# Performance work log

Hardware: AMD Instinct MI355X
Metric: run time of the kernel (lower is better)

The kernel has to match this reference:

```python
import jax, jax.numpy as jnp
import numpy as np

SCALE = 1.0
DENSE = 4
ITERS = 5


def setup_inputs() -> dict:
    key = jax.random.key(0)
    k1, k2, k3 = jax.random.split(key, 3)
    N, C, H, W = 32, 3, 512, 512
    data = jax.random.uniform(k1, (N, C, H, W), dtype=jnp.float32)
    # marginal attention distributions along x (width) and y (height); strictly positive
    attx = jax.random.uniform(k2, (N, W, 1), dtype=jnp.float32) + 1e-3
    atty = jax.random.uniform(k3, (N, H, 1), dtype=jnp.float32) + 1e-3
    return {"data": data, "attx": attx, "atty": atty}


def _iterative_clip(ax, ay, out_size, dense, iters):
    # ax, ay: (N, A) positive marginals. Normalize so each sums to out_size,
    # then iteratively clip peaks to a threshold and redistribute the clipped
    # mass uniformly (the mobula AttSamplerGrid iterative refinement).
    A = ax.shape[1]
    ax = ax / jnp.sum(ax, 1, keepdims=True) * out_size
    ay = ay / jnp.sum(ay, 1, keepdims=True) * out_size
    thr0 = jnp.float32(dense * out_size / A)
    for i in range(iters):
        t = jnp.minimum(jnp.max(ax, 1, keepdims=True), jnp.max(ay, 1, keepdims=True))
        if i == 0:
            t = jnp.minimum(t, thr0)
        ax = jnp.minimum(ax, t)
        ay = jnp.minimum(ay, t)
        ax = ax + (out_size - jnp.sum(ax, 1, keepdims=True)) / A
        ay = ay + (out_size - jnp.sum(ay, 1, keepdims=True)) / A
    return ax, ay


def _inverse_cdf(att, out_size):
    # att: (N, A) density summing (approximately) to out_size.
    # For each of out_size equally-spaced mass targets, find the fractional
    # source index p (piecewise-linear inverse of the cumulative sum), then
    # map p in [0, A] to a normalized grid coordinate in [-1, 1].
    N, A = att.shape
    c = jnp.cumsum(att, axis=1)                               # (N, A)
    step = c[:, -1] / out_size                                # ~1.0 per output pixel
    t = (jnp.arange(out_size, dtype=att.dtype) + 0.5) * step[:, None]  # (N, out)
    j = jax.vmap(lambda cr, tr: jnp.searchsorted(cr, tr, side="left"))(c, t)
    j = jnp.clip(j, 0, A - 1)
    c_prev = jnp.where(j > 0, jnp.take_along_axis(c, jnp.maximum(j - 1, 0), 1), 0.0)
    dens = jnp.take_along_axis(c, j, 1) - c_prev              # = att[n, j]
    p = j.astype(att.dtype) + (t - c_prev) / jnp.maximum(dens, 1e-6)
    return 2.0 * p / A - 1.0                                  # (N, out) in [-1, 1]


def _grid_sample_bilinear(data, grid):
    # data: (N, C, H, W); grid: (N, Ho, Wo, 2) with grid[...,0]=x, grid[...,1]=y
    # in [-1, 1]; bilinear, align_corners=True, border clamp (grid stays in range).
    N, C, H, W = data.shape
    ix = (grid[..., 0] + 1.0) * 0.5 * (W - 1)
    iy = (grid[..., 1] + 1.0) * 0.5 * (H - 1)
    x0 = jnp.floor(ix)
    y0 = jnp.floor(iy)
    wx = ix - x0
    wy = iy - y0
    x0i = jnp.clip(x0.astype(jnp.int32), 0, W - 1)
    x1i = jnp.clip(x0i + 1, 0, W - 1)
    y0i = jnp.clip(y0.astype(jnp.int32), 0, H - 1)
    y1i = jnp.clip(y0i + 1, 0, H - 1)

    def sample_one(img, x0i, x1i, y0i, y1i, wx, wy):
        # img: (C, H, W); index arrays: (Ho, Wo) -> gathers are (C, Ho, Wo)
        v00 = img[:, y0i, x0i]
        v01 = img[:, y0i, x1i]
        v10 = img[:, y1i, x0i]
        v11 = img[:, y1i, x1i]
        top = v00 * (1.0 - wx) + v01 * wx
        bot = v10 * (1.0 - wx) + v11 * wx
        return top * (1.0 - wy) + bot * wy

    return jax.vmap(sample_one)(data, x0i, x1i, y0i, y1i, wx, wy)


def reference(data, attx, atty):
    N, C, H, W = data.shape
    out_size = int(H * SCALE)
    ax, ay = _iterative_clip(attx[:, :, 0], atty[:, :, 0], out_size, DENSE, ITERS)
    px = _inverse_cdf(ax, out_size)   # x coords, vary along width
    py = _inverse_cdf(ay, out_size)   # y coords, vary along height
    gx = jnp.broadcast_to(px[:, None, :], (N, out_size, out_size))
    gy = jnp.broadcast_to(py[:, :, None], (N, out_size, out_size))
    grid = jnp.stack([gx, gy], axis=3)            # (N, Ho, Wo, 2)
    sampled = _grid_sample_bilinear(data, grid)   # (N, C, Ho, Wo)
    return sampled, grid
```

## Files before the change

### kernel.cpp

```cpp
#include <hip/hip_runtime.h>

#define NB   32
#define NC   3
#define HH   512
#define WW   512
#define AA   512
#define OUT  512

__device__ __forceinline__ float wave_sum(float v) {
#pragma unroll
    for (int m = 32; m > 0; m >>= 1) v += __shfl_xor(v, m, 64);
    return v;
}
__device__ __forceinline__ float wave_max(float v) {
#pragma unroll
    for (int m = 32; m > 0; m >>= 1) v = fmaxf(v, __shfl_xor(v, m, 64));
    return v;
}

__device__ __forceinline__ float block_sum(float v, float* red, int tid) {
    v = wave_sum(v);
    if ((tid & 63) == 0) red[tid >> 6] = v;
    __syncthreads();
    float r = red[0];
#pragma unroll
    for (int k = 1; k < 8; ++k) r += red[k];
    __syncthreads();
    return r;
}
__device__ __forceinline__ float block_max(float v, float* red, int tid) {
    v = wave_max(v);
    if ((tid & 63) == 0) red[tid >> 6] = v;
    __syncthreads();
    float r = red[0];
#pragma unroll
    for (int k = 1; k < 8; ++k) r = fmaxf(r, red[k]);
    __syncthreads();
    return r;
}

__global__ __launch_bounds__(512) void clip_cdf_kernel(
    const float* __restrict__ attx, const float* __restrict__ atty,
    float* __restrict__ px, float* __restrict__ py)
{
    __shared__ float red[8];
    __shared__ float cs[AA];

    const int n   = blockIdx.x;
    const int tid = threadIdx.x;

    float ax = attx[n * AA + tid];
    float ay = atty[n * AA + tid];

    float sx = block_sum(ax, red, tid);
    float sy = block_sum(ay, red, tid);
    ax = ax / sx * (float)OUT;
    ay = ay / sy * (float)OUT;

#pragma unroll
    for (int it = 0; it < 5; ++it) {
        float mx = block_max(ax, red, tid);
        float my = block_max(ay, red, tid);
        float tv = fminf(mx, my);
        if (it == 0) tv = fminf(tv, 4.0f);
        ax = fminf(ax, tv);
        ay = fminf(ay, tv);
        float sax = block_sum(ax, red, tid);
        float say = block_sum(ay, red, tid);
        ax += ((float)OUT - sax) * (1.0f / (float)AA);
        ay += ((float)OUT - say) * (1.0f / (float)AA);
    }

#pragma unroll
    for (int which = 0; which < 2; ++which) {
        float v = (which == 0) ? ax : ay;
        cs[tid] = v;
        __syncthreads();
#pragma unroll
        for (int off = 1; off < AA; off <<= 1) {
            float add = (tid >= off) ? cs[tid - off] : 0.0f;
            __syncthreads();
            cs[tid] += add;
            __syncthreads();
        }
        float total = cs[AA - 1];
        float step  = total / (float)OUT;
        float tk    = ((float)tid + 0.5f) * step;

        int lo = 0, hi = AA;
        while (lo < hi) {
            int mid = (lo + hi) >> 1;
            if (cs[mid] < tk) lo = mid + 1; else hi = mid;
        }
        int j = lo; if (j > AA - 1) j = AA - 1;
        float cprev = (j > 0) ? cs[j - 1] : 0.0f;
        float dens  = cs[j] - cprev;
        float p     = (float)j + (tk - cprev) / fmaxf(dens, 1e-6f);
        float g     = 2.0f * p / (float)AA - 1.0f;
        if (which == 0) px[n * OUT + tid] = g;
        else            py[n * OUT + tid] = g;
        __syncthreads();
    }
}

__global__ __launch_bounds__(256) void sample_kernel(
    const float* __restrict__ data, const float* __restrict__ px,
    const float* __restrict__ py, float* __restrict__ sampled,
    float2* __restrict__ grid)
{
    __shared__ float lrow[6][WW];

    const int bid = blockIdx.x;
    const int n   = bid >> 9;
    const int i   = bid & (OUT - 1);

    const float gy  = py[n * OUT + i];
    const float iy  = (gy + 1.0f) * 0.5f * (float)(HH - 1);
    const float y0f = floorf(iy);
    const float wy  = iy - y0f;
    int y0 = (int)y0f;
    y0 = max(0, min(y0, HH - 1));
    const int y1 = min(y0 + 1, HH - 1);

    const float* dbase = data + (size_t)n * NC * HH * WW;

#pragma unroll
    for (int k = 0; k < 3; ++k) {
        const int idx = threadIdx.x + k * 256;
        const int row = idx >> 7;
        const int q   = idx & 127;
        const int c   = (row < 3) ? row : row - 3;
        const int y   = (row < 3) ? y0 : y1;
        const float4 v = ((const float4*)(dbase + ((size_t)c * HH + y) * WW))[q];
        ((float4*)&lrow[row][0])[q] = v;
    }
    __syncthreads();

    float*  sbase = sampled + (size_t)n * NC * HH * WW + (size_t)i * WW;
    float2* gbase = grid + ((size_t)n * OUT + i) * OUT;
    const float omwy = 1.0f - wy;

#pragma unroll
    for (int rep = 0; rep < 2; ++rep) {
        const int j = threadIdx.x + rep * 256;
        const float gx  = px[n * OUT + j];
        const float ix  = (gx + 1.0f) * 0.5f * (float)(WW - 1);
        const float x0f = floorf(ix);
        const float wx  = ix - x0f;
        int x0 = (int)x0f;
        x0 = max(0, min(x0, WW - 1));
        const int x1 = min(x0 + 1, WW - 1);
        const float omwx = 1.0f - wx;

        gbase[j] = make_float2(gx, gy);

#pragma unroll
        for (int c = 0; c < NC; ++c) {
            const float v00 = lrow[c][x0];
            const float v01 = lrow[c][x1];
            const float v10 = lrow[3 + c][x0];
            const float v11 = lrow[3 + c][x1];
            const float top = v00 * omwx + v01 * wx;
            const float bot = v10 * omwx + v11 * wx;
            sbase[(size_t)c * HH * WW + j] = top * omwy + bot * wy;
        }
    }
}

extern "C" void kernel_launch(void* const* d_in, const int* in_sizes, int n_in,
                              void* d_out, int out_size, void* d_ws, size_t ws_size,
                              hipStream_t stream) {
    const float* data = (const float*)d_in[0];
    const float* attx = (const float*)d_in[1];
    const float* atty = (const float*)d_in[2];

    float* px = (float*)d_ws;
    float* py = px + NB * OUT;

    float*  out     = (float*)d_out;
    float*  sampled = out;
    float2* grid    = (float2*)(out + (size_t)NB * NC * HH * WW);

    clip_cdf_kernel<<<NB, 512, 0, stream>>>(attx, atty, px, py);
    sample_kernel<<<NB * OUT, 256, 0, stream>>>(data, px, py, sampled, grid);
}
```

Measured before the change: 253.3 us.

## Fuse x/y reductions, use wave-shuffle scan, vectorize stores, swizzle block order

The clip/CDF kernel now reduces x and y together, halving the number of block barriers. It replaces the barrier-heavy shared-memory Hillis-Steele scan with a wave shuffle-up scan plus a per-wave prefix. The sample kernel handles two adjacent output columns per thread, so the grid and sampled outputs are written with float4/float2 stores. Blocks are remapped so consecutive block IDs are spread across batch images, which may change cache and channel locality. The sample kernel is write-bandwidth bound, so the wider stores matter most, and the remap could help or hurt.

```diff
diff --git a/kernel.cpp b/kernel.cpp
--- a/kernel.cpp
+++ b/kernel.cpp
@@ -7,99 +7,124 @@
 #define AA   512
 #define OUT  512
 
-__device__ __forceinline__ float wave_sum(float v) {
-#pragma unroll
-    for (int m = 32; m > 0; m >>= 1) v += __shfl_xor(v, m, 64);
-    return v;
-}
-__device__ __forceinline__ float wave_max(float v) {
-#pragma unroll
-    for (int m = 32; m > 0; m >>= 1) v = fmaxf(v, __shfl_xor(v, m, 64));
-    return v;
-}
-
-__device__ __forceinline__ float block_sum(float v, float* red, int tid) {
-    v = wave_sum(v);
-    if ((tid & 63) == 0) red[tid >> 6] = v;
-    __syncthreads();
-    float r = red[0];
-#pragma unroll
-    for (int k = 1; k < 8; ++k) r += red[k];
-    __syncthreads();
-    return r;
-}
-__device__ __forceinline__ float block_max(float v, float* red, int tid) {
-    v = wave_max(v);
-    if ((tid & 63) == 0) red[tid >> 6] = v;
-    __syncthreads();
-    float r = red[0];
-#pragma unroll
-    for (int k = 1; k < 8; ++k) r = fmaxf(r, red[k]);
-    __syncthreads();
-    return r;
+__device__ __forceinline__ void wave_sum2(float& x, float& y) {
+#pragma unroll
+    for (int m = 32; m > 0; m >>= 1) {
+        x += __shfl_xor(x, m, 64);
+        y += __shfl_xor(y, m, 64);
+    }
+}
+__device__ __forceinline__ void wave_max2(float& x, float& y) {
+#pragma unroll
+    for (int m = 32; m > 0; m >>= 1) {
+        x = fmaxf(x, __shfl_xor(x, m, 64));
+        y = fmaxf(y, __shfl_xor(y, m, 64));
+    }
+}
+
+__device__ __forceinline__ void block_sum2(float& vx, float& vy,
+                                           float* redx, float* redy, int tid) {
+    wave_sum2(vx, vy);
+    if ((tid & 63) == 0) { redx[tid >> 6] = vx; redy[tid >> 6] = vy; }
+    __syncthreads();
+    float rx = redx[0], ry = redy[0];
+#pragma unroll
+    for (int k = 1; k < 8; ++k) { rx += redx[k]; ry += redy[k]; }
+    __syncthreads();
+    vx = rx; vy = ry;
+}
+__device__ __forceinline__ void block_max2(float& vx, float& vy,
+                                           float* redx, float* redy, int tid) {
+    wave_max2(vx, vy);
+    if ((tid & 63) == 0) { redx[tid >> 6] = vx; redy[tid >> 6] = vy; }
+    __syncthreads();
+    float rx = redx[0], ry = redy[0];
+#pragma unroll
+    for (int k = 1; k < 8; ++k) { rx = fmaxf(rx, redx[k]); ry = fmaxf(ry, redy[k]); }
+    __syncthreads();
+    vx = rx; vy = ry;
 }
 
 __global__ __launch_bounds__(512) void clip_cdf_kernel(
     const float* __restrict__ attx, const float* __restrict__ atty,
     float* __restrict__ px, float* __restrict__ py)
 {
-    __shared__ float red[8];
-    __shared__ float cs[AA];
-
-    const int n   = blockIdx.x;
-    const int tid = threadIdx.x;
+    __shared__ float redx[8], redy[8];
+    __shared__ float csx[AA], csy[AA];
+
+    const int n    = blockIdx.x;
+    const int tid  = threadIdx.x;
+    const int wave = tid >> 6;
+    const int lane = tid & 63;
 
     float ax = attx[n * AA + tid];
     float ay = atty[n * AA + tid];
 
-    float sx = block_sum(ax, red, tid);
-    float sy = block_sum(ay, red, tid);
+    float sx = ax, sy = ay;
+    block_sum2(sx, sy, redx, redy, tid);
     ax = ax / sx * (float)OUT;
     ay = ay / sy * (float)OUT;
 
 #pragma unroll
     for (int it = 0; it < 5; ++it) {
-        float mx = block_max(ax, red, tid);
-        float my = block_max(ay, red, tid);
+        float mx = ax, my = ay;
+        block_max2(mx, my, redx, redy, tid);
         float tv = fminf(mx, my);
         if (it == 0) tv = fminf(tv, 4.0f);
         ax = fminf(ax, tv);
         ay = fminf(ay, tv);
-        float sax = block_sum(ax, red, tid);
-        float say = block_sum(ay, red, tid);
+        float sax = ax, say = ay;
+        block_sum2(sax, say, redx, redy, tid);
         ax += ((float)OUT - sax) * (1.0f / (float)AA);
         ay += ((float)OUT - say) * (1.0f / (float)AA);
     }
 
-#pragma unroll
-    for (int which = 0; which < 2; ++which) {
-        float v = (which == 0) ? ax : ay;
-        cs[tid] = v;
-        __syncthreads();
-#pragma unroll
-        for (int off = 1; off < AA; off <<= 1) {
-            float add = (tid >= off) ? cs[tid - off] : 0.0f;
-            __syncthreads();
-            cs[tid] += add;
-            __syncthreads();
-        }
-        float total = cs[AA - 1];
-        float step  = total / (float)OUT;
-        float tk    = ((float)tid + 0.5f) * step;
-
+    float vsx = ax, vsy = ay;
+#pragma unroll
+    for (int off = 1; off < 64; off <<= 1) {
+        float ux = __shfl_up(vsx, off, 64);
+        float uy = __shfl_up(vsy, off, 64);
+        if (lane >= off) { vsx += ux; vsy += uy; }
+    }
+    if (lane == 63) { redx[wave] = vsx; redy[wave] = vsy; }
+    __syncthreads();
+    float pfx = 0.0f, pfy = 0.0f;
+#pragma unroll
+    for (int k = 0; k < 8; ++k) {
+        if (k < wave) { pfx += redx[k]; pfy += redy[k]; }
+    }
+    csx[tid] = vsx + pfx;
+    csy[tid] = vsy + pfy;
+    __syncthreads();
+
+    const float totx = csx[AA - 1];
+    const float toty = csy[AA - 1];
+    const float tkx  = ((float)tid + 0.5f) * (totx * (1.0f / (float)OUT));
+    const float tky  = ((float)tid + 0.5f) * (toty * (1.0f / (float)OUT));
+
+    {
         int lo = 0, hi = AA;
         while (lo < hi) {
             int mid = (lo + hi) >> 1;
-            if (cs[mid] < tk) lo = mid + 1; else hi = mid;
+            if (csx[mid] < tkx) lo = mid + 1; else hi = mid;
         }
-        int j = lo; if (j > AA - 1) j = AA - 1;
-        float cprev = (j > 0) ? cs[j - 1] : 0.0f;
-        float dens  = cs[j] - cprev;
-        float p     = (float)j + (tk - cprev) / fmaxf(dens, 1e-6f);
-        float g     = 2.0f * p / (float)AA - 1.0f;
-        if (which == 0) px[n * OUT + tid] = g;
-        else            py[n * OUT + tid] = g;
-        __syncthreads();
+        int j = min(lo, AA - 1);
+        float cprev = (j > 0) ? csx[j - 1] : 0.0f;
+        float dens  = csx[j] - cprev;
+        float p     = (float)j + (tkx - cprev) / fmaxf(dens, 1e-6f);
+        px[n * OUT + tid] = 2.0f * p * (1.0f / (float)AA) - 1.0f;
+    }
+    {
+        int lo = 0, hi = AA;
+        while (lo < hi) {
+            int mid = (lo + hi) >> 1;
+            if (csy[mid] < tky) lo = mid + 1; else hi = mid;
+        }
+        int j = min(lo, AA - 1);
+        float cprev = (j > 0) ? csy[j - 1] : 0.0f;
+        float dens  = csy[j] - cprev;
+        float p     = (float)j + (tky - cprev) / fmaxf(dens, 1e-6f);
+        py[n * OUT + tid] = 2.0f * p * (1.0f / (float)AA) - 1.0f;
     }
 }
 
@@ -110,9 +135,10 @@
 {
     __shared__ float lrow[6][WW];
 
-    const int bid = blockIdx.x;
-    const int n   = bid >> 9;
-    const int i   = bid & (OUT - 1);
+    const int d = blockIdx.x;
+    const int g = ((d & 7) << 11) + (d >> 3);
+    const int n = g >> 9;
+    const int i = g & (OUT - 1);
 
     const float gy  = py[n * OUT + i];
     const float iy  = (gy + 1.0f) * 0.5f * (float)(HH - 1);
@@ -136,34 +162,39 @@
     }
     __syncthreads();
 
-    float*  sbase = sampled + (size_t)n * NC * HH * WW + (size_t)i * WW;
-    float2* gbase = grid + ((size_t)n * OUT + i) * OUT;
+    float*  sbase  = sampled + (size_t)n * NC * HH * WW + (size_t)i * WW;
+    float4* gbase4 = (float4*)(grid + ((size_t)n * OUT + i) * OUT);
     const float omwy = 1.0f - wy;
 
-#pragma unroll
-    for (int rep = 0; rep < 2; ++rep) {
-        const int j = threadIdx.x + rep * 256;
-        const float gx  = px[n * OUT + j];
-        const float ix  = (gx + 1.0f) * 0.5f * (float)(WW - 1);
-        const float x0f = floorf(ix);
-        const float wx  = ix - x0f;
-        int x0 = (int)x0f;
-        x0 = max(0, min(x0, WW - 1));
-        const int x1 = min(x0 + 1, WW - 1);
-        const float omwx = 1.0f - wx;
-
-        gbase[j] = make_float2(gx, gy);
-
-#pragma unroll
-        for (int c = 0; c < NC; ++c) {
-            const float v00 = lrow[c][x0];
-            const float v01 = lrow[c][x1];
-            const float v10 = lrow[3 + c][x0];
-            const float v11 = lrow[3 + c][x1];
-            const float top = v00 * omwx + v01 * wx;
-            const float bot = v10 * omwx + v11 * wx;
-            sbase[(size_t)c * HH * WW + j] = top * omwy + bot * wy;
-        }
+    const int t = threadIdx.x;
+    const float2 pxv = ((const float2*)(px + n * OUT))[t];
+
+    const float ixa  = (pxv.x + 1.0f) * 0.5f * (float)(WW - 1);
+    const float x0fa = floorf(ixa);
+    const float wxa  = ixa - x0fa;
+    int x0a = (int)x0fa; x0a = max(0, min(x0a, WW - 1));
+    const int x1a = min(x0a + 1, WW - 1);
+    const float omwxa = 1.0f - wxa;
+    const float ixb  = (pxv.y + 1.0f) * 0.5f * (float)(WW - 1);
+    const float x0fb = floorf(ixb);
+    const float wxb  = ixb - x0fb;
+    int x0b = (int)x0fb; x0b = max(0, min(x0b, WW - 1));
+    const int x1b = min(x0b + 1, WW - 1);
+    const float omwxb = 1.0f - wxb;
+
+    gbase4[t] = make_float4(pxv.x, gy, pxv.y, gy);
+
+#pragma unroll
+    for (int c = 0; c < NC; ++c) {
+        const float* r0 = &lrow[c][0];
+        const float* r1 = &lrow[3 + c][0];
+        const float topa = r0[x0a] * omwxa + r0[x1a] * wxa;
+        const float bota = r1[x0a] * omwxa + r1[x1a] * wxa;
+        const float topb = r0[x0b] * omwxb + r0[x1b] * wxb;
+        const float botb = r1[x0b] * omwxb + r1[x1b] * wxb;
+        const float ra = topa * omwy + bota * wy;
+        const float rb = topb * omwy + botb * wy;
+        ((float2*)(sbase + (size_t)c * HH * WW))[t] = make_float2(ra, rb);
     }
 }
 
```

New measurement: 253.8 us. Within noise of the previous version (+0.2%).
